# Kernel optimization log

Measured on AMD Instinct MI355X. Metric: run time of the kernel, lower is better.

Reference implementation:

```python
import jax, jax.numpy as jnp
import numpy as np

L = 3
EPSILON = 0.01
T = 1.0
L1_EPS = 1e-12  # torch F.normalize default eps


def _cdist(x, y):
    # Euclidean pairwise distance, (b, n, d) x (b, m, d) -> (b, n, m)
    x2 = jnp.sum(x * x, axis=-1, keepdims=True)            # (b, n, 1)
    y2 = jnp.sum(y * y, axis=-1)[:, None, :]               # (b, 1, m)
    xy = jnp.einsum('bnd,bmd->bnm', x, y)                  # (b, n, m)
    return jnp.sqrt(jnp.maximum(x2 + y2 - 2.0 * xy, 0.0))


def setup_inputs() -> dict:
    key = jax.random.key(0)
    k1, k2 = jax.random.split(key)
    B, S, D = 4, 2048, 512
    A = jax.random.uniform(k1, (B, S, S), dtype=jnp.float32)
    V = jax.random.normal(k2, (B, S, D), dtype=jnp.float32)
    return {"A": A, "V": V}


def reference(A, V):
    M = jnp.matmul(A, V)  # (b, s, d)
    for _ in range(L):
        Md = jax.lax.stop_gradient(M)
        Vd = jax.lax.stop_gradient(V)
        dist = _cdist(Md, Vd)                               # (b, s, s)
        w = 1.0 / (dist + EPSILON)                          # norm == 'L2'
        ww = w * A                                          # (b, s, s)
        l1 = jnp.maximum(jnp.sum(jnp.abs(ww), axis=-1, keepdims=True), L1_EPS)
        ww_norm = ww / l1
        M = (1.0 - T) * M + T * jnp.matmul(ww_norm, V)
    return M
```

## Files before the change

### kernel.cpp

```cpp
#include <hip/hip_runtime.h>


typedef __bf16 bf16;
typedef bf16 bf16x4 __attribute__((ext_vector_type(4)));
typedef bf16 bf16x8 __attribute__((ext_vector_type(8)));
typedef float f32x4 __attribute__((ext_vector_type(4)));

#define S_DIM 2048
#define D_DIM 512
#define NB    4
#define EPSILON 0.01f

__global__ void cast_kernel(const float* __restrict__ in, bf16* __restrict__ out, int n4) {
  int i = blockIdx.x * blockDim.x + threadIdx.x;
  if (i >= n4) return;
  float4 v = ((const float4*)in)[i];
  bf16x4 o = { (bf16)v.x, (bf16)v.y, (bf16)v.z, (bf16)v.w };
  ((bf16x4*)out)[i] = o;
}

__global__ void vprep_kernel(const float* __restrict__ V, bf16* __restrict__ Vbf,
                             bf16* __restrict__ Vt, float* __restrict__ v2) {
  __shared__ float tile[64][68];
  int b  = blockIdx.y;
  int r0 = blockIdx.x * 64;
  const float* Vb = V   + (size_t)b * S_DIM * D_DIM;
  bf16*       Vfb = Vbf + (size_t)b * S_DIM * D_DIM;
  bf16*       Vtb = Vt  + (size_t)b * S_DIM * D_DIM;
  float*      v2b = v2  + (size_t)b * S_DIM;
  int tx = threadIdx.x & 15, ty = threadIdx.x >> 4;
  float acc2[4] = { 0.f, 0.f, 0.f, 0.f };
  for (int c = 0; c < 8; ++c) {
    int c0 = c * 64;
#pragma unroll
    for (int i = 0; i < 4; ++i) {
      int r = ty + i * 16;
      float4 v = *(const float4*)(Vb + (size_t)(r0 + r) * D_DIM + (c0 + tx * 4));
      tile[r][tx * 4 + 0] = v.x; tile[r][tx * 4 + 1] = v.y;
      tile[r][tx * 4 + 2] = v.z; tile[r][tx * 4 + 3] = v.w;
      bf16x4 o = { (bf16)v.x, (bf16)v.y, (bf16)v.z, (bf16)v.w };
      *(bf16x4*)(Vfb + (size_t)(r0 + r) * D_DIM + (c0 + tx * 4)) = o;
#pragma unroll
      for (int j = 0; j < 4; ++j) { float f = (float)o[j]; acc2[i] += f * f; }
    }
    __syncthreads();
#pragma unroll
    for (int i = 0; i < 4; ++i) {
      int cc = ty + i * 16;
      bf16x4 o = { (bf16)tile[tx * 4 + 0][cc], (bf16)tile[tx * 4 + 1][cc],
                   (bf16)tile[tx * 4 + 2][cc], (bf16)tile[tx * 4 + 3][cc] };
      *(bf16x4*)(Vtb + (size_t)(c0 + cc) * S_DIM + (r0 + tx * 4)) = o;
    }
    __syncthreads();
  }
#pragma unroll
  for (int i = 0; i < 4; ++i) {
    float s = acc2[i];
    s += __shfl_xor(s, 1); s += __shfl_xor(s, 2);
    s += __shfl_xor(s, 4); s += __shfl_xor(s, 8);
    if (tx == 0) v2b[r0 + ty + i * 16] = s;
  }
}

template <int MODE>
__global__ __launch_bounds__(256, 4)
void gemm_kernel(const bf16* __restrict__ Amat, const bf16* __restrict__ Bmat,
                 int M, int N, int K,
                 bf16* __restrict__ Cp,
                 const float* __restrict__ m2, const float* __restrict__ v2,
                 const bf16* __restrict__ Aw, bf16* __restrict__ Wout,
                 float* __restrict__ l1p) {
  int bz, ks, kbeg, kend;
  if (MODE == 4) { bz = blockIdx.z >> 1; ks = blockIdx.z & 1; kbeg = ks * (K >> 1); kend = kbeg + (K >> 1); }
  else           { bz = blockIdx.z;      ks = 0;              kbeg = 0;             kend = K; }
  const int row0 = blockIdx.y * 128;
  const int col0 = blockIdx.x * 128;
  const bf16* Ab = Amat + (size_t)bz * M * K;
  const bf16* Bb = Bmat + (size_t)bz * N * K;

  __shared__ char smem[33792];
  bf16*  ldsA = (bf16*)smem;
  bf16*  ldsB = (bf16*)(smem + 16384);
  float* ldsW = (float*)smem;

  const int tid  = threadIdx.x;
  const int wave = tid >> 6;
  const int lane = tid & 63;
  const int wr   = wave >> 1;
  const int wc   = wave & 1;
  const int q    = lane >> 4;
  const int c16  = lane & 15;

  const int srow = lane >> 3;
  const int scol = ((lane & 7) ^ srow) * 8;

  f32x4 acc[4][4] = {};

  for (int k0 = kbeg; k0 < kend; k0 += 64) {
#pragma unroll
    for (int i = 0; i < 4; ++i) {
      int slot = wave * 4 + i;
      int r = slot * 8 + srow;
      __builtin_amdgcn_global_load_lds(
          (const __attribute__((address_space(1))) void*)(Ab + (size_t)(row0 + r) * K + (k0 + scol)),
          (__attribute__((address_space(3))) void*)(ldsA + slot * 512), 16, 0, 0);
      __builtin_amdgcn_global_load_lds(
          (const __attribute__((address_space(1))) void*)(Bb + (size_t)(col0 + r) * K + (k0 + scol)),
          (__attribute__((address_space(3))) void*)(ldsB + slot * 512), 16, 0, 0);
    }
    __syncthreads();

#pragma unroll
    for (int kk = 0; kk < 2; ++kk) {
      bf16x8 afr[4], bfr[4];
#pragma unroll
      for (int mt = 0; mt < 4; ++mt) {
        int R = wr * 64 + mt * 16 + c16;
        int p = ((kk << 2) + q) ^ (c16 & 7);
        afr[mt] = *(const bf16x8*)(ldsA + (size_t)R * 64 + p * 8);
      }
#pragma unroll
      for (int nt = 0; nt < 4; ++nt) {
        int R = wc * 64 + nt * 16 + c16;
        int p = ((kk << 2) + q) ^ (c16 & 7);
        bfr[nt] = *(const bf16x8*)(ldsB + (size_t)R * 64 + p * 8);
      }
#pragma unroll
      for (int mt = 0; mt < 4; ++mt)
#pragma unroll
        for (int nt = 0; nt < 4; ++nt)
          acc[mt][nt] = __builtin_amdgcn_mfma_f32_16x16x32_bf16(afr[mt], bfr[nt], acc[mt][nt], 0, 0, 0);
    }
    __syncthreads();
  }

  const int rowBase = row0 + wr * 64 + q * 4;
  const int colBase = col0 + wc * 64 + c16;

  if (MODE == 1) {
    const float* m2b = m2 + (size_t)bz * M;
    const float* v2b = v2 + (size_t)bz * N;
    float v2v[4];
#pragma unroll
    for (int nt = 0; nt < 4; ++nt) v2v[nt] = v2b[colBase + nt * 16];
#pragma unroll
    for (int mt = 0; mt < 4; ++mt)
#pragma unroll
      for (int r = 0; r < 4; ++r) {
        float m2v = m2b[rowBase + mt * 16 + r];
#pragma unroll
        for (int nt = 0; nt < 4; ++nt) {
          float d2 = fmaxf(m2v + v2v[nt] - 2.f * acc[mt][nt][r], 0.f);
          acc[mt][nt][r] = __builtin_amdgcn_rcpf(__builtin_amdgcn_sqrtf(d2) + EPSILON);
        }
      }
  }

  const int lr  = tid >> 3;
  const int sub = tid & 7;
#pragma unroll
  for (int h = 0; h < 2; ++h) {
    __syncthreads();
    if (wr == h) {
#pragma unroll
      for (int mt = 0; mt < 4; ++mt)
#pragma unroll
        for (int nt = 0; nt < 4; ++nt)
#pragma unroll
          for (int r = 0; r < 4; ++r)
            ldsW[(mt * 16 + q * 4 + r) * 132 + wc * 64 + nt * 16 + c16] = acc[mt][nt][r];
    }
    __syncthreads();
#pragma unroll
    for (int h2 = 0; h2 < 2; ++h2) {
      int rloc = lr + 32 * h2;
      int gi = row0 + 64 * h + rloc;
      const float* wp = ldsW + rloc * 132 + sub * 16;
      float4 w0 = *(const float4*)(wp + 0);
      float4 w1 = *(const float4*)(wp + 4);
      float4 w2 = *(const float4*)(wp + 8);
      float4 w3 = *(const float4*)(wp + 12);
      float wv_[16] = { w0.x, w0.y, w0.z, w0.w, w1.x, w1.y, w1.z, w1.w,
                        w2.x, w2.y, w2.z, w2.w, w3.x, w3.y, w3.z, w3.w };
      if (MODE == 1) {
        const bf16* ap = Aw + (size_t)bz * M * N + (size_t)gi * N + (col0 + sub * 16);
        bf16x8 a0 = *(const bf16x8*)(ap);
        bf16x8 a1 = *(const bf16x8*)(ap + 8);
        bf16x8 o0, o1;
        float rs = 0.f;
#pragma unroll
        for (int e = 0; e < 8; ++e) {
          float x0 = wv_[e] * (float)a0[e];
          float x1 = wv_[e + 8] * (float)a1[e];
          o0[e] = (bf16)x0; o1[e] = (bf16)x1;
          rs += fabsf(x0) + fabsf(x1);
        }
        bf16* op = Wout + (size_t)bz * M * N + (size_t)gi * N + (col0 + sub * 16);
        *(bf16x8*)(op)     = o0;
        *(bf16x8*)(op + 8) = o1;
        rs += __shfl_xor(rs, 1);
        rs += __shfl_xor(rs, 2);
        rs += __shfl_xor(rs, 4);
        if (sub == 0) l1p[((size_t)blockIdx.x * NB + bz) * M + gi] = rs;
      } else {
        bf16* Cb = Cp + ((size_t)ks * NB + bz) * ((size_t)M * N);
        bf16x8 o0, o1;
#pragma unroll
        for (int e = 0; e < 8; ++e) { o0[e] = (bf16)wv_[e]; o1[e] = (bf16)wv_[e + 8]; }
        bf16* op = Cb + (size_t)gi * N + (col0 + sub * 16);
        *(bf16x8*)(op)     = o0;
        *(bf16x8*)(op + 8) = o1;
      }
    }
  }
}

template <int RMODE>
__global__ void reduce_kernel(const bf16* __restrict__ part, const float* __restrict__ l1p,
                              bf16* __restrict__ Mo, float* __restrict__ Fo,
                              float* __restrict__ m2) {
  int wave = threadIdx.x >> 6, lane = threadIdx.x & 63;
  int rg = blockIdx.x * 4 + wave;
  const bf16* p0 = part + (size_t)rg * D_DIM + lane * 8;
  const bf16* p1 = p0 + (size_t)NB * S_DIM * D_DIM;
  bf16x8 a = *(const bf16x8*)p0;
  bf16x8 b = *(const bf16x8*)p1;
  float v[8];
#pragma unroll
  for (int e = 0; e < 8; ++e) v[e] = (float)a[e] + (float)b[e];
  float sc = 1.f;
  if (RMODE >= 1) {
    int bb = rg >> 11, row = rg & (S_DIM - 1);
    float l1v = 0.f;
#pragma unroll
    for (int e = 0; e < 16; ++e) l1v += l1p[((size_t)e * NB + bb) * S_DIM + row];
    sc = __builtin_amdgcn_rcpf(fmaxf(l1v, 1e-12f));
  }
  float s = 0.f;
#pragma unroll
  for (int e = 0; e < 8; ++e) { v[e] *= sc; s += v[e] * v[e]; }
  if (RMODE == 2) {
    float4 o0 = { v[0], v[1], v[2], v[3] }, o1 = { v[4], v[5], v[6], v[7] };
    float* op = Fo + (size_t)rg * D_DIM + lane * 8;
    *(float4*)(op) = o0; *(float4*)(op + 4) = o1;
  } else {
    bf16x8 o;
#pragma unroll
    for (int e = 0; e < 8; ++e) o[e] = (bf16)v[e];
    *(bf16x8*)(Mo + (size_t)rg * D_DIM + lane * 8) = o;
#pragma unroll
    for (int off = 32; off > 0; off >>= 1) s += __shfl_xor(s, off);
    if (lane == 0) m2[rg] = s;
  }
}

extern "C" void kernel_launch(void* const* d_in, const int* in_sizes, int n_in,
                              void* d_out, int out_size, void* d_ws, size_t ws_size,
                              hipStream_t stream) {
  const float* A = (const float*)d_in[0];
  const float* V = (const float*)d_in[1];
  float* out = (float*)d_out;

  char* ws = (char*)d_ws;
  bf16* Abf = (bf16*)ws;   ws += (size_t)NB * S_DIM * S_DIM * 2;
  bf16* Vbf = (bf16*)ws;   ws += (size_t)NB * S_DIM * D_DIM * 2;
  bf16* Vt  = (bf16*)ws;   ws += (size_t)NB * S_DIM * D_DIM * 2;
  bf16* Mbf = (bf16*)ws;   ws += (size_t)NB * S_DIM * D_DIM * 2;
  bf16* Wbf = (bf16*)ws;   ws += (size_t)NB * S_DIM * S_DIM * 2;
  bf16* part = (bf16*)ws;  ws += (size_t)2 * NB * S_DIM * D_DIM * 2;
  float* v2 = (float*)ws;  ws += (size_t)NB * S_DIM * 4;
  float* m2 = (float*)ws;  ws += (size_t)NB * S_DIM * 4;
  float* l1p = (float*)ws; ws += (size_t)16 * NB * S_DIM * 4;

  int nA4 = NB * S_DIM * S_DIM / 4;
  cast_kernel<<<nA4 / 256, 256, 0, stream>>>(A, Abf, nA4);
  vprep_kernel<<<dim3(S_DIM / 64, NB), 256, 0, stream>>>(V, Vbf, Vt, v2);

  gemm_kernel<4><<<dim3(D_DIM / 128, S_DIM / 128, NB * 2), 256, 0, stream>>>(
      Abf, Vt, S_DIM, D_DIM, S_DIM, part, nullptr, nullptr, nullptr, nullptr, nullptr);
  reduce_kernel<0><<<NB * S_DIM / 4, 256, 0, stream>>>(part, nullptr, Mbf, nullptr, m2);

  for (int it = 0; it < 3; ++it) {
    gemm_kernel<1><<<dim3(S_DIM / 128, S_DIM / 128, NB), 256, 0, stream>>>(
        Mbf, Vbf, S_DIM, S_DIM, D_DIM, nullptr, m2, v2, Abf, Wbf, l1p);
    gemm_kernel<4><<<dim3(D_DIM / 128, S_DIM / 128, NB * 2), 256, 0, stream>>>(
        Wbf, Vt, S_DIM, D_DIM, S_DIM, part, nullptr, nullptr, nullptr, nullptr, nullptr);
    if (it < 2)
      reduce_kernel<1><<<NB * S_DIM / 4, 256, 0, stream>>>(part, l1p, Mbf, nullptr, m2);
    else
      reduce_kernel<2><<<NB * S_DIM / 4, 256, 0, stream>>>(part, l1p, nullptr, out, nullptr);
  }
}
```

Baseline: 334.2 us.

## Add 256x256-tile distance GEMM kernel with direct-to-LDS double-buffered loads

Replaces the 128x128-tile MODE 1 distance/weight GEMM with a dedicated 512-thread kernel that computes 256x256 output tiles. It stages operands with global_load_lds into a double-buffered shared memory layout and raises wave priority around the MFMA blocks. The larger tile cuts redundant global reads of M and V and halves the number of L1 partial columns (16 to 8), which the reduce kernel now sums. In exchange it uses 128KB LDS and many accumulator registers per thread, and launches only 256 blocks, which lowers occupancy and wave-level parallelism.

```diff
diff --git a/kernel.cpp b/kernel.cpp
--- a/kernel.cpp
+++ b/kernel.cpp
@@ -59,6 +59,155 @@
     s += __shfl_xor(s, 1); s += __shfl_xor(s, 2);
     s += __shfl_xor(s, 4); s += __shfl_xor(s, 8);
     if (tx == 0) v2b[r0 + ty + i * 16] = s;
+  }
+}
+
+__global__ __launch_bounds__(512, 2)
+void gemm256_kernel(const bf16* __restrict__ Amat, const bf16* __restrict__ Bmat,
+                    int M, int N, int K,
+                    const float* __restrict__ m2, const float* __restrict__ v2,
+                    const bf16* __restrict__ Aw, bf16* __restrict__ Wout,
+                    float* __restrict__ l1p) {
+  const int bz   = blockIdx.z;
+  const int row0 = blockIdx.y * 256;
+  const int col0 = blockIdx.x * 256;
+  const bf16* Ab = Amat + (size_t)bz * M * K;
+  const bf16* Bb = Bmat + (size_t)bz * N * K;
+
+  __shared__ bf16 smem[65536];
+
+  const int tid  = threadIdx.x;
+  const int w    = tid >> 6;
+  const int lane = tid & 63;
+  const int wr   = w >> 2;
+  const int wc   = w & 3;
+  const int q    = lane >> 4;
+  const int c16  = lane & 15;
+  const int srow = lane >> 3;
+  const int schk = (lane & 7) ^ srow;
+
+  f32x4 acc[8][4] = {};
+  const int NT = K >> 6;
+
+  auto stageA = [&](int nb, int k0) {
+    bf16* la = smem + nb * 32768;
+#pragma unroll
+    for (int i = 0; i < 4; ++i)
+      __builtin_amdgcn_global_load_lds(
+          (const __attribute__((address_space(1))) void*)(
+              Ab + (size_t)(row0 + i * 64 + w * 8 + srow) * K + (k0 + schk * 8)),
+          (__attribute__((address_space(3))) void*)(la + (i * 64 + w * 8) * 64), 16, 0, 0);
+  };
+  auto stageB = [&](int nb, int k0) {
+    bf16* lb = smem + nb * 32768 + 16384;
+#pragma unroll
+    for (int i = 0; i < 4; ++i)
+      __builtin_amdgcn_global_load_lds(
+          (const __attribute__((address_space(1))) void*)(
+              Bb + (size_t)(col0 + i * 64 + w * 8 + srow) * K + (k0 + schk * 8)),
+          (__attribute__((address_space(3))) void*)(lb + (i * 64 + w * 8) * 64), 16, 0, 0);
+  };
+
+  stageA(0, 0); stageB(0, 0);
+  asm volatile("s_waitcnt vmcnt(0)" ::: "memory");
+  __builtin_amdgcn_s_barrier();
+
+  int cur = 0;
+  for (int t = 0; t < NT; ++t) {
+    const int k0 = t << 6;
+    const bf16* la = smem + cur * 32768;
+    const bf16* lb = la + 16384;
+    if (t + 1 < NT) stageA(cur ^ 1, k0 + 64);
+#pragma unroll
+    for (int kk = 0; kk < 2; ++kk) {
+      bf16x8 afr[8], bfr[4];
+      const int p = ((kk << 2) + q) ^ (c16 & 7);
+#pragma unroll
+      for (int m = 0; m < 8; ++m)
+        afr[m] = *(const bf16x8*)(la + (size_t)(wr * 128 + m * 16 + c16) * 64 + p * 8);
+#pragma unroll
+      for (int n = 0; n < 4; ++n)
+        bfr[n] = *(const bf16x8*)(lb + (size_t)(wc * 64 + n * 16 + c16) * 64 + p * 8);
+      if (kk == 0 && t + 1 < NT) stageB(cur ^ 1, k0 + 64);
+      __builtin_amdgcn_s_setprio(1);
+#pragma unroll
+      for (int m = 0; m < 8; ++m)
+#pragma unroll
+        for (int n = 0; n < 4; ++n)
+          acc[m][n] = __builtin_amdgcn_mfma_f32_16x16x32_bf16(afr[m], bfr[n], acc[m][n], 0, 0, 0);
+      __builtin_amdgcn_s_setprio(0);
+    }
+    asm volatile("s_waitcnt vmcnt(0)" ::: "memory");
+    __builtin_amdgcn_s_barrier();
+    cur ^= 1;
+  }
+
+  const float* m2b = m2 + (size_t)bz * M;
+  const float* v2b = v2 + (size_t)bz * N;
+  float v2v[4];
+#pragma unroll
+  for (int n = 0; n < 4; ++n) v2v[n] = v2b[col0 + wc * 64 + n * 16 + c16];
+#pragma unroll
+  for (int m = 0; m < 8; ++m)
+#pragma unroll
+    for (int r = 0; r < 4; ++r) {
+      float m2v = m2b[row0 + wr * 128 + m * 16 + q * 4 + r];
+#pragma unroll
+      for (int n = 0; n < 4; ++n) {
+        float d2 = fmaxf(m2v + v2v[n] - 2.f * acc[m][n][r], 0.f);
+        acc[m][n][r] = __builtin_amdgcn_rcpf(__builtin_amdgcn_sqrtf(d2) + EPSILON);
+      }
+    }
+
+  float* ldsW = (float*)smem;
+  const int lr  = tid >> 4;
+  const int sub = tid & 15;
+#pragma unroll
+  for (int s = 0; s < 4; ++s) {
+    if (wr == (s >> 1)) {
+      const int mb = (s & 1) * 4;
+#pragma unroll
+      for (int mt = 0; mt < 4; ++mt)
+#pragma unroll
+        for (int n = 0; n < 4; ++n)
+#pragma unroll
+          for (int r = 0; r < 4; ++r)
+            ldsW[(mt * 16 + q * 4 + r) * 268 + wc * 64 + n * 16 + c16] = acc[mb + mt][n][r];
+    }
+    __syncthreads();
+#pragma unroll
+    for (int h2 = 0; h2 < 2; ++h2) {
+      const int rloc = lr + 32 * h2;
+      const int gi = row0 + s * 64 + rloc;
+      const float* wp = ldsW + rloc * 268 + sub * 16;
+      float4 w0 = *(const float4*)(wp + 0);
+      float4 w1 = *(const float4*)(wp + 4);
+      float4 w2 = *(const float4*)(wp + 8);
+      float4 w3 = *(const float4*)(wp + 12);
+      float wv_[16] = { w0.x, w0.y, w0.z, w0.w, w1.x, w1.y, w1.z, w1.w,
+                        w2.x, w2.y, w2.z, w2.w, w3.x, w3.y, w3.z, w3.w };
+      const bf16* ap = Aw + (size_t)bz * M * N + (size_t)gi * N + (col0 + sub * 16);
+      bf16x8 a0 = *(const bf16x8*)(ap);
+      bf16x8 a1 = *(const bf16x8*)(ap + 8);
+      bf16x8 o0, o1;
+      float rs = 0.f;
+#pragma unroll
+      for (int e = 0; e < 8; ++e) {
+        float x0 = wv_[e] * (float)a0[e];
+        float x1 = wv_[e + 8] * (float)a1[e];
+        o0[e] = (bf16)x0; o1[e] = (bf16)x1;
+        rs += fabsf(x0) + fabsf(x1);
+      }
+      bf16* op = Wout + (size_t)bz * M * N + (size_t)gi * N + (col0 + sub * 16);
+      *(bf16x8*)(op)     = o0;
+      *(bf16x8*)(op + 8) = o1;
+      rs += __shfl_xor(rs, 1);
+      rs += __shfl_xor(rs, 2);
+      rs += __shfl_xor(rs, 4);
+      rs += __shfl_xor(rs, 8);
+      if (sub == 0) l1p[((size_t)blockIdx.x * NB + bz) * M + gi] = rs;
+    }
+    __syncthreads();
   }
 }
 
@@ -134,28 +283,6 @@
     __syncthreads();
   }
 
-  const int rowBase = row0 + wr * 64 + q * 4;
-  const int colBase = col0 + wc * 64 + c16;
-
-  if (MODE == 1) {
-    const float* m2b = m2 + (size_t)bz * M;
-    const float* v2b = v2 + (size_t)bz * N;
-    float v2v[4];
-#pragma unroll
-    for (int nt = 0; nt < 4; ++nt) v2v[nt] = v2b[colBase + nt * 16];
-#pragma unroll
-    for (int mt = 0; mt < 4; ++mt)
-#pragma unroll
-      for (int r = 0; r < 4; ++r) {
-        float m2v = m2b[rowBase + mt * 16 + r];
-#pragma unroll
-        for (int nt = 0; nt < 4; ++nt) {
-          float d2 = fmaxf(m2v + v2v[nt] - 2.f * acc[mt][nt][r], 0.f);
-          acc[mt][nt][r] = __builtin_amdgcn_rcpf(__builtin_amdgcn_sqrtf(d2) + EPSILON);
-        }
-      }
-  }
-
   const int lr  = tid >> 3;
   const int sub = tid & 7;
 #pragma unroll
@@ -182,39 +309,19 @@
       float4 w3 = *(const float4*)(wp + 12);
       float wv_[16] = { w0.x, w0.y, w0.z, w0.w, w1.x, w1.y, w1.z, w1.w,
                         w2.x, w2.y, w2.z, w2.w, w3.x, w3.y, w3.z, w3.w };
-      if (MODE == 1) {
-        const bf16* ap = Aw + (size_t)bz * M * N + (size_t)gi * N + (col0 + sub * 16);
-        bf16x8 a0 = *(const bf16x8*)(ap);
-        bf16x8 a1 = *(const bf16x8*)(ap + 8);
-        bf16x8 o0, o1;
-        float rs = 0.f;
-#pragma unroll
-        for (int e = 0; e < 8; ++e) {
-          float x0 = wv_[e] * (float)a0[e];
-          float x1 = wv_[e + 8] * (float)a1[e];
-          o0[e] = (bf16)x0; o1[e] = (bf16)x1;
-          rs += fabsf(x0) + fabsf(x1);
-        }
-        bf16* op = Wout + (size_t)bz * M * N + (size_t)gi * N + (col0 + sub * 16);
-        *(bf16x8*)(op)     = o0;
-        *(bf16x8*)(op + 8) = o1;
-        rs += __shfl_xor(rs, 1);
-        rs += __shfl_xor(rs, 2);
-        rs += __shfl_xor(rs, 4);
-        if (sub == 0) l1p[((size_t)blockIdx.x * NB + bz) * M + gi] = rs;
-      } else {
-        bf16* Cb = Cp + ((size_t)ks * NB + bz) * ((size_t)M * N);
-        bf16x8 o0, o1;
-#pragma unroll
-        for (int e = 0; e < 8; ++e) { o0[e] = (bf16)wv_[e]; o1[e] = (bf16)wv_[e + 8]; }
-        bf16* op = Cb + (size_t)gi * N + (col0 + sub * 16);
-        *(bf16x8*)(op)     = o0;
-        *(bf16x8*)(op + 8) = o1;
-      }
-    }
-  }
-}
-
+      bf16* Cb = Cp + ((size_t)ks * NB + bz) * ((size_t)M * N);
+      bf16x8 o0, o1;
+#pragma unroll
+      for (int e = 0; e < 8; ++e) { o0[e] = (bf16)wv_[e]; o1[e] = (bf16)wv_[e + 8]; }
+      bf16* op = Cb + (size_t)gi * N + (col0 + sub * 16);
+      *(bf16x8*)(op)     = o0;
+      *(bf16x8*)(op + 8) = o1;
+    }
+  }
+}
+
+__global__ void reduce_kernel_0(const bf16* __restrict__ part,
+                                bf16* __restrict__ Mo, float* __restrict__ m2);
 template <int RMODE>
 __global__ void reduce_kernel(const bf16* __restrict__ part, const float* __restrict__ l1p,
                               bf16* __restrict__ Mo, float* __restrict__ Fo,
@@ -233,7 +340,7 @@
     int bb = rg >> 11, row = rg & (S_DIM - 1);
     float l1v = 0.f;
 #pragma unroll
-    for (int e = 0; e < 16; ++e) l1v += l1p[((size_t)e * NB + bb) * S_DIM + row];
+    for (int e = 0; e < 8; ++e) l1v += l1p[((size_t)e * NB + bb) * S_DIM + row];
     sc = __builtin_amdgcn_rcpf(fmaxf(l1v, 1e-12f));
   }
   float s = 0.f;
@@ -281,8 +388,8 @@
   reduce_kernel<0><<<NB * S_DIM / 4, 256, 0, stream>>>(part, nullptr, Mbf, nullptr, m2);
 
   for (int it = 0; it < 3; ++it) {
-    gemm_kernel<1><<<dim3(S_DIM / 128, S_DIM / 128, NB), 256, 0, stream>>>(
-        Mbf, Vbf, S_DIM, S_DIM, D_DIM, nullptr, m2, v2, Abf, Wbf, l1p);
+    gemm256_kernel<<<dim3(S_DIM / 256, S_DIM / 256, NB), 512, 0, stream>>>(
+        Mbf, Vbf, S_DIM, S_DIM, D_DIM, m2, v2, Abf, Wbf, l1p);
     gemm_kernel<4><<<dim3(D_DIM / 128, S_DIM / 128, NB * 2), 256, 0, stream>>>(
         Wbf, Vt, S_DIM, D_DIM, S_DIM, part, nullptr, nullptr, nullptr, nullptr, nullptr);
     if (it < 2)
```

New measurement: 350.5 us. 4.9% more time.

## Fuse distance GEMM, weighting and second GEMM into one flash-style kernel

Applied to the files above, without the earlier changes.

Replaces the per-iteration pair of GEMMs (M·V^T producing a bf16 weight matrix in global memory, then W·V) with a single fused kernel. Each block holds a 64-row M tile in LDS, computes 128-column distance tiles, applies the inverse distance and A weighting in registers, and writes the weights to LDS where they feed the second MFMA GEMM directly. A split of the j dimension in two produces partial outputs and L1 sums. This removes the global write and read of the S×S weight matrix, at the cost of heavy LDS use (128 KB per block), lower occupancy, and manual barrier and waitcnt synchronisation.

```diff
diff --git a/kernel.cpp b/kernel.cpp
--- a/kernel.cpp
+++ b/kernel.cpp
@@ -10,6 +10,9 @@
 #define D_DIM 512
 #define NB    4
 #define EPSILON 0.01f
+
+#define AS1 __attribute__((address_space(1)))
+#define AS3 __attribute__((address_space(3)))
 
 __global__ void cast_kernel(const float* __restrict__ in, bf16* __restrict__ out, int n4) {
   int i = blockIdx.x * blockDim.x + threadIdx.x;
@@ -59,6 +62,210 @@
     s += __shfl_xor(s, 1); s += __shfl_xor(s, 2);
     s += __shfl_xor(s, 4); s += __shfl_xor(s, 8);
     if (tx == 0) v2b[r0 + ty + i * 16] = s;
+  }
+}
+
+__global__ __launch_bounds__(512, 2)
+void fused_kernel(const bf16* __restrict__ Mbf, const bf16* __restrict__ Vbf,
+                  const bf16* __restrict__ Vt, const bf16* __restrict__ Abf,
+                  const float* __restrict__ m2, const float* __restrict__ v2,
+                  bf16* __restrict__ part, float* __restrict__ l1p) {
+  const int b  = blockIdx.z;
+  const int i0 = blockIdx.y * 64;
+  const int js = blockIdx.x;
+  const int jbase = js * 1024;
+
+  const bf16* Mb = Mbf + (size_t)b * S_DIM * D_DIM;
+  const bf16* Vb = Vbf + (size_t)b * S_DIM * D_DIM;
+  const bf16* Tb = Vt  + (size_t)b * S_DIM * D_DIM;
+  const bf16* Ab = Abf + (size_t)b * S_DIM * S_DIM;
+  const float* m2b = m2 + (size_t)b * S_DIM;
+  const float* v2b = v2 + (size_t)b * S_DIM;
+
+  __shared__ bf16 smem[65536];
+  bf16* Mlds = smem;
+  bf16* B1   = smem + 32768;
+  bf16* Wt   = smem + 32768;
+  bf16* Bt   = smem + 49152;
+  float* l1lds = (float*)(smem + 32768);
+  float* slab  = (float*)(smem + 49152);
+
+  const int tid  = threadIdx.x;
+  const int w    = tid >> 6;
+  const int lane = tid & 63;
+  const int pr   = w >> 1;
+  const int pc   = w & 1;
+  const int q    = lane >> 4;
+  const int c16  = lane & 15;
+  const int x7   = c16 & 7;
+  const int srow  = lane >> 3;
+  const int schk  = (lane & 7) ^ srow;
+  const int srow4 = lane >> 4;
+  const int lchk  = lane & 15;
+
+  f32x4 acc2[16] = {};
+  float l1acc[4] = { 0.f, 0.f, 0.f, 0.f };
+  uint4 btr[4];
+
+#pragma unroll
+  for (int kt = 0; kt < 8; ++kt)
+    __builtin_amdgcn_global_load_lds(
+        (const AS1 void*)(Mb + (size_t)(i0 + w * 8 + srow) * D_DIM + kt * 64 + schk * 8),
+        (AS3 void*)(Mlds + kt * 4096 + w * 512), 16, 0, 0);
+
+  float m2v[4];
+#pragma unroll
+  for (int r = 0; r < 4; ++r) m2v[r] = m2b[i0 + pr * 16 + q * 4 + r];
+
+  for (int jt = 0; jt < 8; ++jt) {
+    const int j0 = jbase + jt * 128;
+    __builtin_amdgcn_s_barrier();
+
+#pragma unroll
+    for (int it = 0; it < 2; ++it)
+      __builtin_amdgcn_global_load_lds(
+          (const AS1 void*)(Vb + (size_t)(j0 + it * 64 + w * 8 + srow) * D_DIM + schk * 8),
+          (AS3 void*)(B1 + (it * 64 + w * 8) * 64), 16, 0, 0);
+#pragma unroll
+    for (int it = 0; it < 4; ++it) {
+      int row = it * 32 + w * 4 + srow4;
+      btr[it] = *(const uint4*)(Tb + (size_t)row * S_DIM + j0 + lchk * 8);
+    }
+
+    f32x4 acc1[4] = {};
+    for (int kt = 0; kt < 8; ++kt) {
+      const int rb = kt & 1;
+      asm volatile("s_waitcnt vmcnt(0)" ::: "memory");
+      __builtin_amdgcn_s_barrier();
+      if (kt < 7) {
+#pragma unroll
+        for (int it = 0; it < 2; ++it)
+          __builtin_amdgcn_global_load_lds(
+              (const AS1 void*)(Vb + (size_t)(j0 + it * 64 + w * 8 + srow) * D_DIM + (kt + 1) * 64 + schk * 8),
+              (AS3 void*)(B1 + (rb ^ 1) * 8192 + (it * 64 + w * 8) * 64), 16, 0, 0);
+      }
+      const bf16* lb = B1 + rb * 8192;
+      __builtin_amdgcn_s_setprio(1);
+#pragma unroll
+      for (int kk = 0; kk < 2; ++kk) {
+        const int p = ((kk << 2) + q) ^ x7;
+        bf16x8 af = *(const bf16x8*)(Mlds + kt * 4096 + (pr * 16 + c16) * 64 + p * 8);
+#pragma unroll
+        for (int n2 = 0; n2 < 4; ++n2) {
+          bf16x8 bv = *(const bf16x8*)(lb + (pc * 64 + n2 * 16 + c16) * 64 + p * 8);
+          acc1[n2] = __builtin_amdgcn_mfma_f32_16x16x32_bf16(af, bv, acc1[n2], 0, 0, 0);
+        }
+      }
+      __builtin_amdgcn_s_setprio(0);
+    }
+
+    float v2v[4];
+#pragma unroll
+    for (int n2 = 0; n2 < 4; ++n2) v2v[n2] = v2b[j0 + pc * 64 + n2 * 16 + c16];
+#pragma unroll
+    for (int n2 = 0; n2 < 4; ++n2)
+#pragma unroll
+      for (int r = 0; r < 4; ++r) {
+        const int rr = pr * 16 + q * 4 + r;
+        const int jl = pc * 64 + n2 * 16 + c16;
+        float d2 = fmaxf(m2v[r] + v2v[n2] - 2.f * acc1[n2][r], 0.f);
+        float w_ = __builtin_amdgcn_rcpf(__builtin_amdgcn_sqrtf(d2) + EPSILON);
+        float a  = (float)Ab[(size_t)(i0 + rr) * S_DIM + j0 + jl];
+        float x  = w_ * a;
+        l1acc[r] += fabsf(x);
+        Wt[rr * 128 + (((jl >> 3) ^ (rr & 7)) << 3) + (jl & 7)] = (bf16)x;
+      }
+#pragma unroll
+    for (int it = 0; it < 4; ++it) {
+      int row = it * 32 + w * 4 + srow4;
+      *(uint4*)(Bt + row * 128 + ((lchk ^ (row & 7)) << 3)) = btr[it];
+    }
+#pragma unroll
+    for (int it = 0; it < 4; ++it) {
+      int row = it * 32 + w * 4 + srow4;
+      btr[it] = *(const uint4*)(Tb + (size_t)(128 + row) * S_DIM + j0 + lchk * 8);
+    }
+    asm volatile("s_waitcnt lgkmcnt(0)" ::: "memory");
+    __builtin_amdgcn_s_barrier();
+
+#pragma unroll
+    for (int ch = 0; ch < 4; ++ch) {
+      __builtin_amdgcn_s_setprio(1);
+#pragma unroll
+      for (int kk = 0; kk < 4; ++kk) {
+        const int p = ((kk << 2) + q) ^ x7;
+        bf16x8 aw = *(const bf16x8*)(Wt + (pr * 16 + c16) * 128 + p * 8);
+#pragma unroll
+        for (int n = 0; n < 4; ++n) {
+          bf16x8 bv = *(const bf16x8*)(Bt + (pc * 64 + n * 16 + c16) * 128 + p * 8);
+          acc2[ch * 4 + n] = __builtin_amdgcn_mfma_f32_16x16x32_bf16(aw, bv, acc2[ch * 4 + n], 0, 0, 0);
+        }
+      }
+      __builtin_amdgcn_s_setprio(0);
+      if (ch < 3) {
+        __builtin_amdgcn_s_barrier();
+        asm volatile("s_waitcnt vmcnt(0)" ::: "memory");
+#pragma unroll
+        for (int it = 0; it < 4; ++it) {
+          int row = it * 32 + w * 4 + srow4;
+          *(uint4*)(Bt + row * 128 + ((lchk ^ (row & 7)) << 3)) = btr[it];
+        }
+        if (ch < 2) {
+#pragma unroll
+          for (int it = 0; it < 4; ++it) {
+            int row = it * 32 + w * 4 + srow4;
+            btr[it] = *(const uint4*)(Tb + (size_t)((ch + 2) * 128 + row) * S_DIM + j0 + lchk * 8);
+          }
+        }
+        asm volatile("s_waitcnt lgkmcnt(0)" ::: "memory");
+        __builtin_amdgcn_s_barrier();
+      }
+    }
+  }
+
+  __builtin_amdgcn_s_barrier();
+#pragma unroll
+  for (int r = 0; r < 4; ++r) {
+    float s = l1acc[r];
+    s += __shfl_xor(s, 1); s += __shfl_xor(s, 2);
+    s += __shfl_xor(s, 4); s += __shfl_xor(s, 8);
+    if (c16 == 0) l1lds[pc * 64 + pr * 16 + q * 4 + r] = s;
+  }
+  asm volatile("s_waitcnt lgkmcnt(0)" ::: "memory");
+  __builtin_amdgcn_s_barrier();
+  if (tid < 64)
+    l1p[((size_t)js * NB + b) * S_DIM + i0 + tid] = l1lds[tid] + l1lds[64 + tid];
+
+  bf16* pp = part + ((size_t)js * NB + b) * (size_t)S_DIM * D_DIM;
+#pragma unroll
+  for (int g = 0; g < 4; ++g) {
+    __builtin_amdgcn_s_barrier();
+    if (pr == g) {
+#pragma unroll
+      for (int ch = 0; ch < 4; ++ch)
+#pragma unroll
+        for (int n = 0; n < 4; ++n)
+#pragma unroll
+          for (int r = 0; r < 4; ++r)
+            slab[(q * 4 + r) * 512 + ch * 128 + pc * 64 + n * 16 + c16] = acc2[ch * 4 + n][r];
+    }
+    asm volatile("s_waitcnt lgkmcnt(0)" ::: "memory");
+    __builtin_amdgcn_s_barrier();
+    {
+      const int row = tid >> 5, col = (tid & 31) * 16;
+      const float* sp = slab + row * 512 + col;
+      float4 f0 = *(const float4*)(sp + 0);
+      float4 f1 = *(const float4*)(sp + 4);
+      float4 f2 = *(const float4*)(sp + 8);
+      float4 f3 = *(const float4*)(sp + 12);
+      bf16x8 o0 = { (bf16)f0.x, (bf16)f0.y, (bf16)f0.z, (bf16)f0.w,
+                    (bf16)f1.x, (bf16)f1.y, (bf16)f1.z, (bf16)f1.w };
+      bf16x8 o1 = { (bf16)f2.x, (bf16)f2.y, (bf16)f2.z, (bf16)f2.w,
+                    (bf16)f3.x, (bf16)f3.y, (bf16)f3.z, (bf16)f3.w };
+      bf16* op = pp + (size_t)(i0 + g * 16 + row) * D_DIM + col;
+      *(bf16x8*)(op)     = o0;
+      *(bf16x8*)(op + 8) = o1;
+    }
   }
 }
 
@@ -102,11 +309,11 @@
       int slot = wave * 4 + i;
       int r = slot * 8 + srow;
       __builtin_amdgcn_global_load_lds(
-          (const __attribute__((address_space(1))) void*)(Ab + (size_t)(row0 + r) * K + (k0 + scol)),
-          (__attribute__((address_space(3))) void*)(ldsA + slot * 512), 16, 0, 0);
+          (const AS1 void*)(Ab + (size_t)(row0 + r) * K + (k0 + scol)),
+          (AS3 void*)(ldsA + slot * 512), 16, 0, 0);
       __builtin_amdgcn_global_load_lds(
-          (const __attribute__((address_space(1))) void*)(Bb + (size_t)(col0 + r) * K + (k0 + scol)),
-          (__attribute__((address_space(3))) void*)(ldsB + slot * 512), 16, 0, 0);
+          (const AS1 void*)(Bb + (size_t)(col0 + r) * K + (k0 + scol)),
+          (AS3 void*)(ldsB + slot * 512), 16, 0, 0);
     }
     __syncthreads();
 
@@ -132,28 +339,6 @@
           acc[mt][nt] = __builtin_amdgcn_mfma_f32_16x16x32_bf16(afr[mt], bfr[nt], acc[mt][nt], 0, 0, 0);
     }
     __syncthreads();
-  }
-
-  const int rowBase = row0 + wr * 64 + q * 4;
-  const int colBase = col0 + wc * 64 + c16;
-
-  if (MODE == 1) {
-    const float* m2b = m2 + (size_t)bz * M;
-    const float* v2b = v2 + (size_t)bz * N;
-    float v2v[4];
-#pragma unroll
-    for (int nt = 0; nt < 4; ++nt) v2v[nt] = v2b[colBase + nt * 16];
-#pragma unroll
-    for (int mt = 0; mt < 4; ++mt)
-#pragma unroll
-      for (int r = 0; r < 4; ++r) {
-        float m2v = m2b[rowBase + mt * 16 + r];
-#pragma unroll
-        for (int nt = 0; nt < 4; ++nt) {
-          float d2 = fmaxf(m2v + v2v[nt] - 2.f * acc[mt][nt][r], 0.f);
-          acc[mt][nt][r] = __builtin_amdgcn_rcpf(__builtin_amdgcn_sqrtf(d2) + EPSILON);
-        }
-      }
   }
 
   const int lr  = tid >> 3;
@@ -182,35 +367,13 @@
       float4 w3 = *(const float4*)(wp + 12);
       float wv_[16] = { w0.x, w0.y, w0.z, w0.w, w1.x, w1.y, w1.z, w1.w,
                         w2.x, w2.y, w2.z, w2.w, w3.x, w3.y, w3.z, w3.w };
-      if (MODE == 1) {
-        const bf16* ap = Aw + (size_t)bz * M * N + (size_t)gi * N + (col0 + sub * 16);
-        bf16x8 a0 = *(const bf16x8*)(ap);
-        bf16x8 a1 = *(const bf16x8*)(ap + 8);
-        bf16x8 o0, o1;
-        float rs = 0.f;
-#pragma unroll
-        for (int e = 0; e < 8; ++e) {
-          float x0 = wv_[e] * (float)a0[e];
-          float x1 = wv_[e + 8] * (float)a1[e];
-          o0[e] = (bf16)x0; o1[e] = (bf16)x1;
-          rs += fabsf(x0) + fabsf(x1);
-        }
-        bf16* op = Wout + (size_t)bz * M * N + (size_t)gi * N + (col0 + sub * 16);
-        *(bf16x8*)(op)     = o0;
-        *(bf16x8*)(op + 8) = o1;
-        rs += __shfl_xor(rs, 1);
-        rs += __shfl_xor(rs, 2);
-        rs += __shfl_xor(rs, 4);
-        if (sub == 0) l1p[((size_t)blockIdx.x * NB + bz) * M + gi] = rs;
-      } else {
-        bf16* Cb = Cp + ((size_t)ks * NB + bz) * ((size_t)M * N);
-        bf16x8 o0, o1;
-#pragma unroll
-        for (int e = 0; e < 8; ++e) { o0[e] = (bf16)wv_[e]; o1[e] = (bf16)wv_[e + 8]; }
-        bf16* op = Cb + (size_t)gi * N + (col0 + sub * 16);
-        *(bf16x8*)(op)     = o0;
-        *(bf16x8*)(op + 8) = o1;
-      }
+      bf16* Cb = Cp + ((size_t)ks * NB + bz) * ((size_t)M * N);
+      bf16x8 o0, o1;
+#pragma unroll
+      for (int e = 0; e < 8; ++e) { o0[e] = (bf16)wv_[e]; o1[e] = (bf16)wv_[e + 8]; }
+      bf16* op = Cb + (size_t)gi * N + (col0 + sub * 16);
+      *(bf16x8*)(op)     = o0;
+      *(bf16x8*)(op + 8) = o1;
     }
   }
 }
@@ -233,7 +396,7 @@
     int bb = rg >> 11, row = rg & (S_DIM - 1);
     float l1v = 0.f;
 #pragma unroll
-    for (int e = 0; e < 16; ++e) l1v += l1p[((size_t)e * NB + bb) * S_DIM + row];
+    for (int e = 0; e < 2; ++e) l1v += l1p[((size_t)e * NB + bb) * S_DIM + row];
     sc = __builtin_amdgcn_rcpf(fmaxf(l1v, 1e-12f));
   }
   float s = 0.f;
@@ -266,11 +429,10 @@
   bf16* Vbf = (bf16*)ws;   ws += (size_t)NB * S_DIM * D_DIM * 2;
   bf16* Vt  = (bf16*)ws;   ws += (size_t)NB * S_DIM * D_DIM * 2;
   bf16* Mbf = (bf16*)ws;   ws += (size_t)NB * S_DIM * D_DIM * 2;
-  bf16* Wbf = (bf16*)ws;   ws += (size_t)NB * S_DIM * S_DIM * 2;
   bf16* part = (bf16*)ws;  ws += (size_t)2 * NB * S_DIM * D_DIM * 2;
   float* v2 = (float*)ws;  ws += (size_t)NB * S_DIM * 4;
   float* m2 = (float*)ws;  ws += (size_t)NB * S_DIM * 4;
-  float* l1p = (float*)ws; ws += (size_t)16 * NB * S_DIM * 4;
+  float* l1p = (float*)ws; ws += (size_t)2 * NB * S_DIM * 4;
 
   int nA4 = NB * S_DIM * S_DIM / 4;
   cast_kernel<<<nA4 / 256, 256, 0, stream>>>(A, Abf, nA4);
@@ -281,10 +443,8 @@
   reduce_kernel<0><<<NB * S_DIM / 4, 256, 0, stream>>>(part, nullptr, Mbf, nullptr, m2);
 
   for (int it = 0; it < 3; ++it) {
-    gemm_kernel<1><<<dim3(S_DIM / 128, S_DIM / 128, NB), 256, 0, stream>>>(
-        Mbf, Vbf, S_DIM, S_DIM, D_DIM, nullptr, m2, v2, Abf, Wbf, l1p);
-    gemm_kernel<4><<<dim3(D_DIM / 128, S_DIM / 128, NB * 2), 256, 0, stream>>>(
-        Wbf, Vt, S_DIM, D_DIM, S_DIM, part, nullptr, nullptr, nullptr, nullptr, nullptr);
+    fused_kernel<<<dim3(2, S_DIM / 64, NB), 512, 0, stream>>>(
+        Mbf, Vbf, Vt, Abf, m2, v2, part, l1p);
     if (it < 2)
       reduce_kernel<1><<<NB * S_DIM / 4, 256, 0, stream>>>(part, l1p, Mbf, nullptr, m2);
     else
```

After: 435.1 us. 30.2% more time.
